# Kernel optimization log

Hardware: AMD Instinct MI355X
Metric: run time of the kernel (lower is better)

Reference implementation:

```python
import jax, jax.numpy as jnp
import numpy as np

N_CLASSES = 128
N_SUPPORT = 5
N_QUERIES = 15  # 20 - n_support, per the hard-coded 20 in the source
D_FEAT = 8192
K = 20
EPS = float(np.finfo(np.float64).eps)  # np.finfo(float).eps in source


def setup_inputs() -> dict:
    key = jax.random.key(0)
    k1, k2, k3 = jax.random.split(key, 3)
    N = N_CLASSES * (N_SUPPORT + N_QUERIES)
    feats = jax.random.normal(k1, (N, D_FEAT), dtype=jnp.float32)  # sigma-normalized pooled embeddings
    s_labels_idx = jax.random.randint(k2, (N_CLASSES * N_SUPPORT,), 0, N_CLASSES, dtype=jnp.int32)
    q_labels_idx = jax.random.randint(k3, (N_CLASSES * N_QUERIES,), 0, N_CLASSES, dtype=jnp.int32)
    alpha = jnp.ones((1,), dtype=jnp.float32) * 0.99
    return {"feats": feats, "alpha": alpha, "s_labels_idx": s_labels_idx,
            "q_labels_idx": q_labels_idx, "k": K}


def reference(feats, alpha, s_labels_idx, q_labels_idx, k):
    N, d = feats.shape
    # W[i,j] = exp(-mean((f_i - f_j)^2) / 2), computed via GEMM expansion
    sq = jnp.sum(feats * feats, axis=1)                      # [N]
    dist = (sq[:, None] + sq[None, :] - 2.0 * feats @ feats.T) / d
    W = jnp.exp(-dist / 2.0)                                 # [N, N]
    # top-k per row, scatter-mask, symmetrize (mask + mask.T > 0)
    _, idx = jax.lax.top_k(W, k)                             # [N, k]
    mask = jnp.zeros_like(W).at[jnp.arange(N)[:, None], idx].set(1.0)
    mask = ((mask + mask.T) > 0).astype(jnp.float32)
    W = W * mask
    # symmetric degree normalization S = D^-1/2 W D^-1/2
    D = W.sum(0)
    dsi = jnp.sqrt(1.0 / (D + EPS))
    S = dsi[:, None] * W * dsi[None, :]
    # closed-form label propagation: F = (I - alpha*S + eps)^-1 @ y
    ys = jax.nn.one_hot(s_labels_idx, N_CLASSES, dtype=jnp.float32)
    yu = jnp.zeros((N_CLASSES * N_QUERIES, N_CLASSES), dtype=jnp.float32)
    y = jnp.concatenate([ys, yu], axis=0)                    # [N, C]
    A = jnp.eye(N, dtype=jnp.float32) - alpha[0] * S + EPS   # scalar eps broadcast, as in source
    F_ = jnp.linalg.inv(A) @ y                               # [N, C]
    # cross-entropy over all rows with ground-truth class indices
    gt = jnp.concatenate([s_labels_idx, q_labels_idx], axis=0)
    logp = jax.nn.log_softmax(F_, axis=1)
    loss = -jnp.mean(jnp.take_along_axis(logp, gt[:, None].astype(jnp.int32), axis=1))
    # query accuracy
    Fq = F_[N_CLASSES * N_SUPPORT:, :]
    acc = jnp.mean((jnp.argmax(Fq, axis=1) == q_labels_idx).astype(jnp.float32))
    return loss, acc
```

## Files before the change

### kernel.cpp

```cpp
#include <hip/hip_runtime.h>
#include <hip/hip_fp8.h>
#include <stdint.h>

#define N 2560
#define NSUP 640
#define NQ 1920
#define NCLS 128
#define DF 8192
#define CAP 1024
#define TITER 8
#define EPSF 2.220446049250313e-16f

typedef __attribute__((ext_vector_type(4))) float f32x4;

__device__ __forceinline__ unsigned short f2bf(float f) {
  unsigned u = __float_as_uint(f);
  return (unsigned short)((u + 0x7FFFu + ((u >> 16) & 1u)) >> 16);
}
__device__ __forceinline__ float bf2f(unsigned short h) {
  return __uint_as_float(((unsigned)h) << 16);
}
__device__ __forceinline__ unsigned char f2e4m3(float f) {
  __hip_fp8_e4m3 h(f);
  return (unsigned char)h.__x;
}
__device__ __forceinline__ unsigned sortkey(float f) {
  unsigned u = __float_as_uint(f);
  return (u & 0x80000000u) ? ~u : (u | 0x80000000u);
}
__device__ __forceinline__ void load_lds16(const void* g, void* l) {
  __builtin_amdgcn_global_load_lds((const __attribute__((address_space(1))) void*)g,
                                   (__attribute__((address_space(3))) void*)l, 16, 0, 0);
}

__global__ void k_prep(const float* __restrict__ feats, unsigned char* __restrict__ fb8,
                       float* __restrict__ sq, const float* __restrict__ alpha,
                       float* __restrict__ rho_tab) {
  int i = blockIdx.x, t = threadIdx.x;
  const float4* src = (const float4*)(feats + (size_t)i * DF);
  uchar4* dst = (uchar4*)(fb8 + (size_t)i * DF);
  float s = 0.f;
#pragma unroll
  for (int it = 0; it < 8; ++it) {
    float4 v = src[it * 256 + t];
    s = fmaf(v.x, v.x, s); s = fmaf(v.y, v.y, s);
    s = fmaf(v.z, v.z, s); s = fmaf(v.w, v.w, s);
    uchar4 o; o.x = f2e4m3(v.x); o.y = f2e4m3(v.y); o.z = f2e4m3(v.z); o.w = f2e4m3(v.w);
    dst[it * 256 + t] = o;
  }
  __shared__ float red[256];
  red[t] = s; __syncthreads();
  for (int o = 128; o > 0; o >>= 1) { if (t < o) red[t] += red[t + o]; __syncthreads(); }
  if (t == 0) sq[i] = red[0];
  if (i == 0 && t == 0) {
    float a = alpha[0];
    float rho = a; rho_tab[0] = rho;
    for (int k2 = 1; k2 < 128; ++k2) { rho = 1.f / (2.f / a - rho); rho_tab[k2] = rho; }
  }
}

__global__ __launch_bounds__(256, 2) void k_gemm(const unsigned char* __restrict__ fb8,
                                                 unsigned short* __restrict__ C0,
                                                 unsigned short* __restrict__ C1,
                                                 unsigned short* __restrict__ C2) {
  __shared__ __align__(16) unsigned char As[2][128 * 64];
  __shared__ __align__(16) unsigned char Bs[2][128 * 64];
  int bid = blockIdx.x;
  int ks = (bid >= 210) + (bid >= 420);
  int tid2 = bid - 210 * ks;
  unsigned short* Cd = (ks == 0) ? C0 : (ks == 1 ? C1 : C2);
  const int kbase = ks * 2752;
  const int kend = kbase + (ks < 2 ? 2752 : 2688);
  int bx = (int)((sqrtf(8.0f * (float)tid2 + 1.0f) - 1.0f) * 0.5f);
  while ((bx + 1) * (bx + 2) / 2 <= tid2) ++bx;
  while (bx * (bx + 1) / 2 > tid2) --bx;
  int by = tid2 - bx * (bx + 1) / 2;
  const int rA = by * 128, rB = bx * 128;
  const int t = threadIdx.x, w = t >> 6, l = t & 63;
  const int q = l >> 4, m = l & 15;
  const int wr = w >> 1, wc = w & 1;
  f32x4 acc[4][4];
#pragma unroll
  for (int a2 = 0; a2 < 4; ++a2)
#pragma unroll
    for (int b2 = 0; b2 < 4; ++b2) acc[a2][b2] = (f32x4){0.f, 0.f, 0.f, 0.f};

  const int u0 = (w * 2 + 0) * 64 + l;
  const int u1 = (w * 2 + 1) * 64 + l;
  const int row0 = (u0 >> 1) & 127;
  const int ko0 = ((u0 >> 8) << 5) + ((((u0 & 1) ^ ((u0 >> 3) & 1))) << 4);
  const int row1 = (u1 >> 1) & 127;
  const int ko1 = ((u1 >> 8) << 5) + ((((u1 & 1) ^ ((u1 >> 3) & 1))) << 4);
  const int so0 = (w * 2 + 0) * 1024;
  const int so1 = (w * 2 + 1) * 1024;
  const int qoff = ((((q >> 1) ^ ((m >> 2) & 1))) << 4) + ((q & 1) << 3);

  const size_t gA0 = (size_t)(rA + row0) * DF + ko0;
  const size_t gA1 = (size_t)(rA + row1) * DF + ko1;
  const size_t gB0 = (size_t)(rB + row0) * DF + ko0;
  const size_t gB1 = (size_t)(rB + row1) * DF + ko1;

#define STAGE(K0, BUF)                                                  \
  do {                                                                  \
    load_lds16(fb8 + gA0 + (K0), (char*)As[BUF] + so0);                 \
    load_lds16(fb8 + gA1 + (K0), (char*)As[BUF] + so1);                 \
    load_lds16(fb8 + gB0 + (K0), (char*)Bs[BUF] + so0);                 \
    load_lds16(fb8 + gB1 + (K0), (char*)Bs[BUF] + so1);                 \
  } while (0)

  STAGE(kbase, 0);
  asm volatile("s_waitcnt vmcnt(0)" ::: "memory");
  __syncthreads();
  int cur = 0;
  for (int k0 = kbase; k0 < kend; k0 += 64) {
    if (k0 + 64 < kend) STAGE(k0 + 64, cur ^ 1);
    const unsigned char* Ab = As[cur];
    const unsigned char* Bb = Bs[cur];
#pragma unroll
    for (int s2 = 0; s2 < 2; ++s2) {
      long long af[4], bv[4];
#pragma unroll
      for (int im = 0; im < 4; ++im)
        af[im] = *(const long long*)(Ab + s2 * 4096 + (wr * 64 + im * 16 + m) * 32 + qoff);
#pragma unroll
      for (int in = 0; in < 4; ++in)
        bv[in] = *(const long long*)(Bb + s2 * 4096 + (wc * 64 + in * 16 + m) * 32 + qoff);
#pragma unroll
      for (int im = 0; im < 4; ++im)
#pragma unroll
        for (int in = 0; in < 4; ++in)
          acc[im][in] = __builtin_amdgcn_mfma_f32_16x16x32_fp8_fp8(
              (long)af[im], (long)bv[in], acc[im][in], 0, 0, 0);
    }
    asm volatile("s_waitcnt vmcnt(0)" ::: "memory");
    __syncthreads();
    cur ^= 1;
  }
#undef STAGE
#pragma unroll
  for (int im = 0; im < 4; ++im) {
    int row0w = rA + wr * 64 + im * 16 + q * 4;
#pragma unroll
    for (int in = 0; in < 4; ++in) {
      int col = rB + wc * 64 + in * 16 + m;
#pragma unroll
      for (int rg = 0; rg < 4; ++rg) {
        unsigned short h = f2bf(acc[im][in][rg]);
        Cd[(size_t)(row0w + rg) * N + col] = h;
        Cd[(size_t)col * N + row0w + rg] = h;
      }
    }
  }
}

__global__ void k_topk(const unsigned short* __restrict__ C0,
                       const unsigned short* __restrict__ C1,
                       const unsigned short* __restrict__ C2,
                       const float* __restrict__ sq, unsigned* __restrict__ M,
                       unsigned* __restrict__ MT) {
  int i = blockIdx.x * 4 + (threadIdx.x >> 6);
  int lane = threadIdx.x & 63;
  const unsigned short* r0 = C0 + (size_t)i * N;
  const unsigned short* r1 = C1 + (size_t)i * N;
  const unsigned short* r2 = C2 + (size_t)i * N;
  unsigned kk[40];
#pragma unroll
  for (int s = 0; s < 40; ++s) {
    int j = lane + (s << 6);
    float c = bf2f(r0[j]) + bf2f(r1[j]) + bf2f(r2[j]);
    kk[s] = sortkey(2.f * c - sq[j]);
  }
  unsigned long long removed = 0ull;
  unsigned myj = 0u;
  for (int t = 0; t < 20; ++t) {
    unsigned bk = 0u; int bs = -1;
#pragma unroll
    for (int s = 0; s < 40; ++s)
      if (!((removed >> s) & 1ull) && kk[s] > bk) { bk = kk[s]; bs = s; }
    unsigned long long packed = (bs < 0) ? 0ull
        : ((((unsigned long long)bk) << 32) |
           (unsigned long long)(0xFFFFFFFFu - (unsigned)(lane + (bs << 6))));
#pragma unroll
    for (int off2 = 32; off2 > 0; off2 >>= 1) {
      unsigned long long o = __shfl_xor(packed, off2, 64);
      if (o > packed) packed = o;
    }
    unsigned jw = 0xFFFFFFFFu - (unsigned)(packed & 0xFFFFFFFFull);
    if ((int)(jw & 63u) == lane) removed |= 1ull << (jw >> 6);
    if (t == lane) myj = jw;
  }
  if (lane < 20) {
    atomicOr(&M[(size_t)i * 80 + (myj >> 5)], 1u << (myj & 31u));
    atomicOr(&MT[(size_t)myj * 80 + (i >> 5)], 1u << (i & 31u));
  }
}

__global__ void k_csr(const unsigned short* __restrict__ C0,
                      const unsigned short* __restrict__ C1,
                      const unsigned short* __restrict__ C2,
                      const float* __restrict__ sq,
                      const unsigned* __restrict__ M, const unsigned* __restrict__ MT,
                      unsigned* __restrict__ csrG,
                      int* __restrict__ degG, float* __restrict__ dsi) {
  int i = blockIdx.x, t = threadIdx.x;
  __shared__ unsigned Mrow[80];
  __shared__ unsigned MTrow[80];
  __shared__ int degs;
  __shared__ unsigned packs[CAP];
  __shared__ float red[256];
  if (t < 80) Mrow[t] = M[(size_t)i * 80 + t];
  if (t >= 128 && t < 208) MTrow[t - 128] = MT[(size_t)i * 80 + (t - 128)];
  if (t == 0) degs = 0;
  __syncthreads();
  const unsigned short* r0c = C0 + (size_t)i * N;
  const unsigned short* r1c = C1 + (size_t)i * N;
  const unsigned short* r2c = C2 + (size_t)i * N;
  float sqi = sq[i];
  float dsum = 0.f;
#pragma unroll
  for (int s = 0; s < 10; ++s) {
    int j = t + (s << 8);
    unsigned mm = (Mrow[j >> 5] | MTrow[j >> 5]) >> (j & 31);
    if (mm & 1u) {
      float c = bf2f(r0c[j]) + bf2f(r1c[j]) + bf2f(r2c[j]);
      float wv = expf((2.f * c - sqi - sq[j]) * (1.f / 16384.f));
      int sl = atomicAdd(&degs, 1);
      if (sl < CAP) packs[sl] = (((unsigned)f2bf(wv)) << 16) | (unsigned)j;
      dsum += wv;
    }
  }
  red[t] = dsum; __syncthreads();
  for (int o = 128; o > 0; o >>= 1) { if (t < o) red[t] += red[t + o]; __syncthreads(); }
  if (t == 0) {
    degG[i] = degs > CAP ? CAP : degs;
    dsi[i] = 1.f / sqrtf(red[0] + EPSF);
  }
  __syncthreads();
  int dgc = degs > CAP ? CAP : degs;
  for (int sl = t; sl < dgc; sl += 256)
    csrG[(size_t)i * CAP + sl] = packs[sl];
}

__global__ void k_scale_init(unsigned* __restrict__ csrG, const int* __restrict__ degG,
                             const float* __restrict__ dsi, const int* __restrict__ slab,
                             float* __restrict__ x, float* __restrict__ r,
                             unsigned short* __restrict__ d0) {
  int i = blockIdx.x * 4 + (threadIdx.x >> 6);
  int lane = threadIdx.x & 63;
  float di = dsi[i];
  int dg = degG[i];
  for (int s = lane; s < dg; s += 64) {
    unsigned p = csrG[(size_t)i * CAP + s];
    int j = p & 0xFFFFu;
    float wv = __uint_as_float(p & 0xFFFF0000u);
    wv *= di * dsi[j];
    csrG[(size_t)i * CAP + s] = (((unsigned)f2bf(wv)) << 16) | (unsigned)j;
  }
  int c0 = 2 * lane;
  float y0 = 0.f, y1 = 0.f;
  if (i < NSUP) {
    int lbl = slab[i];
    y0 = (lbl == c0) ? 1.f : 0.f;
    y1 = (lbl == c0 + 1) ? 1.f : 0.f;
  }
  size_t o = (size_t)i * NCLS + c0;
  x[o] = 0.f; x[o + 1] = 0.f;
  r[o] = y0;  r[o + 1] = y1;
  ushort2 dini; dini.x = f2bf(y0); dini.y = f2bf(y1);
  *(ushort2*)(d0 + o) = dini;
}

__global__ __launch_bounds__(256) void k_cheby(const unsigned* __restrict__ csrG,
                        const int* __restrict__ degG, const float* __restrict__ rho_tab,
                        const float* __restrict__ alpha, float* __restrict__ x,
                        float* __restrict__ r, const unsigned short* __restrict__ dcur,
                        unsigned short* __restrict__ dnxt, int it) {
  int i = blockIdx.x;
  int t = threadIdx.x;
  int g4 = (t & 31) << 2, p = t >> 5;
  __shared__ unsigned lcv[CAP];
  __shared__ float4 partial[256];
  int dg = degG[i];
  for (int s = t; s < dg; s += 256) lcv[s] = csrG[(size_t)i * CAP + s];
  __syncthreads();
  float4 acc = make_float4(0.f, 0.f, 0.f, 0.f);
  int s = p;
  for (; s + 56 < dg; s += 64) {
    unsigned uu[8]; ushort4 a[8];
#pragma unroll
    for (int u = 0; u < 8; ++u) {
      uu[u] = lcv[s + 8 * u];
      a[u] = *(const ushort4*)(dcur + (size_t)(uu[u] & 0xFFFFu) * NCLS + g4);
    }
#pragma unroll
    for (int u = 0; u < 8; ++u) {
      float v = __uint_as_float(uu[u] & 0xFFFF0000u);
      acc.x = fmaf(v, bf2f(a[u].x), acc.x);
      acc.y = fmaf(v, bf2f(a[u].y), acc.y);
      acc.z = fmaf(v, bf2f(a[u].z), acc.z);
      acc.w = fmaf(v, bf2f(a[u].w), acc.w);
    }
  }
  for (; s < dg; s += 8) {
    unsigned uu = lcv[s];
    ushort4 a = *(const ushort4*)(dcur + (size_t)(uu & 0xFFFFu) * NCLS + g4);
    float v = __uint_as_float(uu & 0xFFFF0000u);
    acc.x = fmaf(v, bf2f(a.x), acc.x); acc.y = fmaf(v, bf2f(a.y), acc.y);
    acc.z = fmaf(v, bf2f(a.z), acc.z); acc.w = fmaf(v, bf2f(a.w), acc.w);
  }
  partial[t] = acc;
  __syncthreads();
  for (int off = 128; off >= 32; off >>= 1) {
    if (t < off) {
      float4 o = partial[t + off];
      float4 m = partial[t];
      m.x += o.x; m.y += o.y; m.z += o.z; m.w += o.w;
      partial[t] = m;
    }
    __syncthreads();
  }
  if (t < 32) {
    float4 ax = partial[t];
    float ahat = alpha[0];
    float rho = rho_tab[it], rhon = rho_tab[it + 1];
    float cc1 = rhon * rho, cc2 = 2.f * rhon / ahat;
    size_t o = (size_t)i * NCLS + 4 * t;
    ushort4 dv = *(const ushort4*)(dcur + o);
    float4 di; di.x = bf2f(dv.x); di.y = bf2f(dv.y); di.z = bf2f(dv.z); di.w = bf2f(dv.w);
    float4 xv = *(float4*)(x + o);
    float4 rv = *(float4*)(r + o);
    float4 q;
    q.x = di.x - ahat * ax.x; q.y = di.y - ahat * ax.y;
    q.z = di.z - ahat * ax.z; q.w = di.w - ahat * ax.w;
    xv.x += di.x; xv.y += di.y; xv.z += di.z; xv.w += di.w;
    rv.x -= q.x; rv.y -= q.y; rv.z -= q.z; rv.w -= q.w;
    ushort4 dn;
    dn.x = f2bf(cc1 * di.x + cc2 * rv.x); dn.y = f2bf(cc1 * di.y + cc2 * rv.y);
    dn.z = f2bf(cc1 * di.z + cc2 * rv.z); dn.w = f2bf(cc1 * di.w + cc2 * rv.w);
    *(float4*)(x + o) = xv;
    *(float4*)(r + o) = rv;
    *(ushort4*)(dnxt + o) = dn;
  }
}

__global__ void k_loss(const float* __restrict__ F, const int* __restrict__ slab,
                       const int* __restrict__ qlab, float* __restrict__ lossSum,
                       int* __restrict__ accCnt) {
  int i = blockIdx.x * 4 + (threadIdx.x >> 6);
  int lane = threadIdx.x & 63;
  int c0 = 2 * lane;
  float2 f = *(const float2*)(F + (size_t)i * NCLS + c0);
  float mx = fmaxf(f.x, f.y);
  for (int o2 = 32; o2 > 0; o2 >>= 1) mx = fmaxf(mx, __shfl_xor(mx, o2, 64));
  float se = expf(f.x - mx) + expf(f.y - mx);
  for (int o2 = 32; o2 > 0; o2 >>= 1) se += __shfl_xor(se, o2, 64);
  float lse = mx + logf(se);
  int gt = (i < NSUP) ? slab[i] : qlab[i - NSUP];
  float fg = ((c0 == gt) ? f.x : 0.f) + ((c0 + 1 == gt) ? f.y : 0.f);
  for (int o2 = 32; o2 > 0; o2 >>= 1) fg += __shfl_xor(fg, o2, 64);
  if (lane == 0) atomicAdd(lossSum, fg - lse);
  if (i >= NSUP) {
    float bvv; int bc;
    if (f.y > f.x) { bvv = f.y; bc = c0 + 1; } else { bvv = f.x; bc = c0; }
    unsigned long long packed =
        (((unsigned long long)sortkey(bvv)) << 32) | (unsigned long long)(unsigned)(127 - bc);
    for (int o2 = 32; o2 > 0; o2 >>= 1) {
      unsigned long long o = __shfl_xor(packed, o2, 64);
      if (o > packed) packed = o;
    }
    int cw = 127 - (int)(packed & 0xFFFFFFFFull);
    if (lane == 0 && cw == qlab[i - NSUP]) atomicAdd(accCnt, 1);
  }
}

__global__ void k_final(const float* __restrict__ lossSum, const int* __restrict__ accCnt,
                        float* __restrict__ out) {
  out[0] = -lossSum[0] / (float)N;
  out[1] = (float)accCnt[0] / (float)NQ;
}

extern "C" void kernel_launch(void* const* d_in, const int* in_sizes, int n_in,
                              void* d_out, int out_size, void* d_ws, size_t ws_size,
                              hipStream_t stream) {
  const float* feats = (const float*)d_in[0];
  const float* alpha = (const float*)d_in[1];
  const int* slab = (const int*)d_in[2];
  const int* qlab = (const int*)d_in[3];
  float* out = (float*)d_out;
  char* ws = (char*)d_ws;

  unsigned short* C0 = (unsigned short*)(ws + 0);
  unsigned short* C1 = (unsigned short*)(ws + 13107200);
  unsigned short* C2 = (unsigned short*)(ws + 26214400);
  float* x           = (float*)(ws + 0);
  float* r           = (float*)(ws + 1310720);
  unsigned short* d0 = (unsigned short*)(ws + 2621440);
  unsigned short* d1 = (unsigned short*)(ws + 3276800);
  unsigned* M   = (unsigned*)(ws + 39321600);
  float* ctrl   = (float*)(ws + 40140800);
  float* lossSum = ctrl;
  int* accCnt   = (int*)(ctrl + 1);
  float* rho_tab = ctrl + 4;
  float* sq     = (float*)(ws + 40141824);
  float* dsi    = (float*)(ws + 40152064);
  int* degG     = (int*)(ws + 40162304);
  unsigned char* fb8 = (unsigned char*)(ws + 40172544);
  unsigned* csrG = (unsigned*)(ws + 40172544);
  unsigned* MT  = (unsigned*)(ws + 50658304);

  hipMemsetAsync(ws + 39321600, 0, 820224, stream);
  k_prep<<<N, 256, 0, stream>>>(feats, fb8, sq, alpha, rho_tab);
  k_gemm<<<630, 256, 0, stream>>>(fb8, C0, C1, C2);
  hipMemsetAsync(ws + 50658304, 0, 819200, stream);
  k_topk<<<N / 4, 256, 0, stream>>>(C0, C1, C2, sq, M, MT);
  k_csr<<<N, 256, 0, stream>>>(C0, C1, C2, sq, M, MT, csrG, degG, dsi);
  k_scale_init<<<N / 4, 256, 0, stream>>>(csrG, degG, dsi, slab, x, r, d0);
  for (int it = 0; it < TITER; ++it) {
    const unsigned short* dc = (it & 1) ? d1 : d0;
    unsigned short* dn = (it & 1) ? d0 : d1;
    k_cheby<<<N, 256, 0, stream>>>(csrG, degG, rho_tab, alpha, x, r, dc, dn, it);
  }
  k_loss<<<N / 4, 256, 0, stream>>>(x, slab, qlab, lossSum, accCnt);
  k_final<<<1, 1, 0, stream>>>(lossSum, accCnt, out);
}
```

Before: 382.7 us.

## Drop split-K GEMM and use shuffle reduction in Chebyshev SpMM

Removes the three-way split-K in the FP8 Gram GEMM, so 210 blocks each cover the full 8192-long K instead of 630 blocks writing three partial bf16 matrices. Top-k and CSR building then read a single C matrix instead of summing three. Separately, the Chebyshev SpMM kernel remaps threads to 8 lanes per 4-column group and reduces with warp shuffles instead of an LDS tree with several barriers. The GEMM now launches fewer blocks than a 256-CU GPU can hold, which lowers GEMM parallelism in exchange for less partial-result traffic and summing.

```diff
diff --git a/kernel.cpp b/kernel.cpp
--- a/kernel.cpp
+++ b/kernel.cpp
@@ -60,17 +60,10 @@
 }
 
 __global__ __launch_bounds__(256, 2) void k_gemm(const unsigned char* __restrict__ fb8,
-                                                 unsigned short* __restrict__ C0,
-                                                 unsigned short* __restrict__ C1,
-                                                 unsigned short* __restrict__ C2) {
+                                                 unsigned short* __restrict__ C) {
   __shared__ __align__(16) unsigned char As[2][128 * 64];
   __shared__ __align__(16) unsigned char Bs[2][128 * 64];
-  int bid = blockIdx.x;
-  int ks = (bid >= 210) + (bid >= 420);
-  int tid2 = bid - 210 * ks;
-  unsigned short* Cd = (ks == 0) ? C0 : (ks == 1 ? C1 : C2);
-  const int kbase = ks * 2752;
-  const int kend = kbase + (ks < 2 ? 2752 : 2688);
+  int tid2 = blockIdx.x;
   int bx = (int)((sqrtf(8.0f * (float)tid2 + 1.0f) - 1.0f) * 0.5f);
   while ((bx + 1) * (bx + 2) / 2 <= tid2) ++bx;
   while (bx * (bx + 1) / 2 > tid2) --bx;
@@ -108,12 +101,12 @@
     load_lds16(fb8 + gB1 + (K0), (char*)Bs[BUF] + so1);                 \
   } while (0)
 
-  STAGE(kbase, 0);
+  STAGE(0, 0);
   asm volatile("s_waitcnt vmcnt(0)" ::: "memory");
   __syncthreads();
   int cur = 0;
-  for (int k0 = kbase; k0 < kend; k0 += 64) {
-    if (k0 + 64 < kend) STAGE(k0 + 64, cur ^ 1);
+  for (int k0 = 0; k0 < DF; k0 += 64) {
+    if (k0 + 64 < DF) STAGE(k0 + 64, cur ^ 1);
     const unsigned char* Ab = As[cur];
     const unsigned char* Bb = Bs[cur];
 #pragma unroll
@@ -146,29 +139,24 @@
 #pragma unroll
       for (int rg = 0; rg < 4; ++rg) {
         unsigned short h = f2bf(acc[im][in][rg]);
-        Cd[(size_t)(row0w + rg) * N + col] = h;
-        Cd[(size_t)col * N + row0w + rg] = h;
+        C[(size_t)(row0w + rg) * N + col] = h;
+        C[(size_t)col * N + row0w + rg] = h;
       }
     }
   }
 }
 
-__global__ void k_topk(const unsigned short* __restrict__ C0,
-                       const unsigned short* __restrict__ C1,
-                       const unsigned short* __restrict__ C2,
+__global__ void k_topk(const unsigned short* __restrict__ C,
                        const float* __restrict__ sq, unsigned* __restrict__ M,
                        unsigned* __restrict__ MT) {
   int i = blockIdx.x * 4 + (threadIdx.x >> 6);
   int lane = threadIdx.x & 63;
-  const unsigned short* r0 = C0 + (size_t)i * N;
-  const unsigned short* r1 = C1 + (size_t)i * N;
-  const unsigned short* r2 = C2 + (size_t)i * N;
+  const unsigned short* r0 = C + (size_t)i * N;
   unsigned kk[40];
 #pragma unroll
   for (int s = 0; s < 40; ++s) {
     int j = lane + (s << 6);
-    float c = bf2f(r0[j]) + bf2f(r1[j]) + bf2f(r2[j]);
-    kk[s] = sortkey(2.f * c - sq[j]);
+    kk[s] = sortkey(2.f * bf2f(r0[j]) - sq[j]);
   }
   unsigned long long removed = 0ull;
   unsigned myj = 0u;
@@ -195,9 +183,7 @@
   }
 }
 
-__global__ void k_csr(const unsigned short* __restrict__ C0,
-                      const unsigned short* __restrict__ C1,
-                      const unsigned short* __restrict__ C2,
+__global__ void k_csr(const unsigned short* __restrict__ C,
                       const float* __restrict__ sq,
                       const unsigned* __restrict__ M, const unsigned* __restrict__ MT,
                       unsigned* __restrict__ csrG,
@@ -212,9 +198,7 @@
   if (t >= 128 && t < 208) MTrow[t - 128] = MT[(size_t)i * 80 + (t - 128)];
   if (t == 0) degs = 0;
   __syncthreads();
-  const unsigned short* r0c = C0 + (size_t)i * N;
-  const unsigned short* r1c = C1 + (size_t)i * N;
-  const unsigned short* r2c = C2 + (size_t)i * N;
+  const unsigned short* r0c = C + (size_t)i * N;
   float sqi = sq[i];
   float dsum = 0.f;
 #pragma unroll
@@ -222,8 +206,7 @@
     int j = t + (s << 8);
     unsigned mm = (Mrow[j >> 5] | MTrow[j >> 5]) >> (j & 31);
     if (mm & 1u) {
-      float c = bf2f(r0c[j]) + bf2f(r1c[j]) + bf2f(r2c[j]);
-      float wv = expf((2.f * c - sqi - sq[j]) * (1.f / 16384.f));
+      float wv = expf((2.f * bf2f(r0c[j]) - sqi - sq[j]) * (1.f / 16384.f));
       int sl = atomicAdd(&degs, 1);
       if (sl < CAP) packs[sl] = (((unsigned)f2bf(wv)) << 16) | (unsigned)j;
       dsum += wv;
@@ -277,23 +260,22 @@
                         unsigned short* __restrict__ dnxt, int it) {
   int i = blockIdx.x;
   int t = threadIdx.x;
-  int g4 = (t & 31) << 2, p = t >> 5;
+  int g4 = (t >> 3) << 2, p = t & 7;
   __shared__ unsigned lcv[CAP];
-  __shared__ float4 partial[256];
   int dg = degG[i];
   for (int s = t; s < dg; s += 256) lcv[s] = csrG[(size_t)i * CAP + s];
   __syncthreads();
   float4 acc = make_float4(0.f, 0.f, 0.f, 0.f);
   int s = p;
-  for (; s + 56 < dg; s += 64) {
-    unsigned uu[8]; ushort4 a[8];
-#pragma unroll
-    for (int u = 0; u < 8; ++u) {
+  for (; s + 24 < dg; s += 32) {
+    unsigned uu[4]; ushort4 a[4];
+#pragma unroll
+    for (int u = 0; u < 4; ++u) {
       uu[u] = lcv[s + 8 * u];
       a[u] = *(const ushort4*)(dcur + (size_t)(uu[u] & 0xFFFFu) * NCLS + g4);
     }
 #pragma unroll
-    for (int u = 0; u < 8; ++u) {
+    for (int u = 0; u < 4; ++u) {
       float v = __uint_as_float(uu[u] & 0xFFFF0000u);
       acc.x = fmaf(v, bf2f(a[u].x), acc.x);
       acc.y = fmaf(v, bf2f(a[u].y), acc.y);
@@ -308,30 +290,25 @@
     acc.x = fmaf(v, bf2f(a.x), acc.x); acc.y = fmaf(v, bf2f(a.y), acc.y);
     acc.z = fmaf(v, bf2f(a.z), acc.z); acc.w = fmaf(v, bf2f(a.w), acc.w);
   }
-  partial[t] = acc;
-  __syncthreads();
-  for (int off = 128; off >= 32; off >>= 1) {
-    if (t < off) {
-      float4 o = partial[t + off];
-      float4 m = partial[t];
-      m.x += o.x; m.y += o.y; m.z += o.z; m.w += o.w;
-      partial[t] = m;
-    }
-    __syncthreads();
-  }
-  if (t < 32) {
-    float4 ax = partial[t];
+#pragma unroll
+  for (int off = 1; off < 8; off <<= 1) {
+    acc.x += __shfl_xor(acc.x, off, 64);
+    acc.y += __shfl_xor(acc.y, off, 64);
+    acc.z += __shfl_xor(acc.z, off, 64);
+    acc.w += __shfl_xor(acc.w, off, 64);
+  }
+  if (p == 0) {
     float ahat = alpha[0];
     float rho = rho_tab[it], rhon = rho_tab[it + 1];
     float cc1 = rhon * rho, cc2 = 2.f * rhon / ahat;
-    size_t o = (size_t)i * NCLS + 4 * t;
+    size_t o = (size_t)i * NCLS + g4;
     ushort4 dv = *(const ushort4*)(dcur + o);
     float4 di; di.x = bf2f(dv.x); di.y = bf2f(dv.y); di.z = bf2f(dv.z); di.w = bf2f(dv.w);
     float4 xv = *(float4*)(x + o);
     float4 rv = *(float4*)(r + o);
     float4 q;
-    q.x = di.x - ahat * ax.x; q.y = di.y - ahat * ax.y;
-    q.z = di.z - ahat * ax.z; q.w = di.w - ahat * ax.w;
+    q.x = di.x - ahat * acc.x; q.y = di.y - ahat * acc.y;
+    q.z = di.z - ahat * acc.z; q.w = di.w - ahat * acc.w;
     xv.x += di.x; xv.y += di.y; xv.z += di.z; xv.w += di.w;
     rv.x -= q.x; rv.y -= q.y; rv.z -= q.z; rv.w -= q.w;
     ushort4 dn;
@@ -389,9 +366,7 @@
   float* out = (float*)d_out;
   char* ws = (char*)d_ws;
 
-  unsigned short* C0 = (unsigned short*)(ws + 0);
-  unsigned short* C1 = (unsigned short*)(ws + 13107200);
-  unsigned short* C2 = (unsigned short*)(ws + 26214400);
+  unsigned short* C = (unsigned short*)(ws + 0);
   float* x           = (float*)(ws + 0);
   float* r           = (float*)(ws + 1310720);
   unsigned short* d0 = (unsigned short*)(ws + 2621440);
@@ -410,10 +385,10 @@
 
   hipMemsetAsync(ws + 39321600, 0, 820224, stream);
   k_prep<<<N, 256, 0, stream>>>(feats, fb8, sq, alpha, rho_tab);
-  k_gemm<<<630, 256, 0, stream>>>(fb8, C0, C1, C2);
+  k_gemm<<<210, 256, 0, stream>>>(fb8, C);
   hipMemsetAsync(ws + 50658304, 0, 819200, stream);
-  k_topk<<<N / 4, 256, 0, stream>>>(C0, C1, C2, sq, M, MT);
-  k_csr<<<N, 256, 0, stream>>>(C0, C1, C2, sq, M, MT, csrG, degG, dsi);
+  k_topk<<<N / 4, 256, 0, stream>>>(C, sq, M, MT);
+  k_csr<<<N, 256, 0, stream>>>(C, sq, M, MT, csrG, degG, dsi);
   k_scale_init<<<N / 4, 256, 0, stream>>>(csrG, degG, dsi, slab, x, r, d0);
   for (int it = 0; it < TITER; ++it) {
     const unsigned short* dc = (it & 1) ? d1 : d0;
```

Result: slower. 494.8 us (+29.3%).
